# Performance work log

Hardware: AMD Instinct MI355X
Metric: run time of the kernel (lower is better)

Reference implementation:

```python
import jax, jax.numpy as jnp
import numpy as np

DIM = 512
HEADS = 8
DIM_HEAD = 64
INNER = HEADS * DIM_HEAD  # 512
PATCH = 64
M = 3
IN_CH = PATCH * PATCH // 2      # 2048
OUT_CH = IN_CH // 2             # 1024
B, N = 8, PATCH * PATCH // 4    # 8, 1024
SCALE = DIM_HEAD ** -0.5


def setup_inputs() -> dict:
    key = jax.random.key(0)
    ks = jax.random.split(key, 16)
    rn = lambda k, shp, s: (jax.random.normal(k, shp, dtype=jnp.float32) * s)
    inp = rn(ks[0], (B, N, DIM), 1.0)
    x = rn(ks[1], (B, N, DIM), 1.0)
    y = rn(ks[2], (B, N, DIM), 1.0)
    # Linear params (torch convention: W [out, in], y = x @ W.T + b)
    Wq = rn(ks[3], (INNER, DIM), DIM ** -0.5)
    bq = jnp.zeros((INNER,), jnp.float32)
    Wkv = rn(ks[4], (2 * INNER, DIM), DIM ** -0.5)
    bkv = jnp.zeros((2 * INNER,), jnp.float32)
    Wf = rn(ks[5], (OUT_CH + M, IN_CH + M), (IN_CH + M) ** -0.5)
    bf = jnp.zeros((OUT_CH + M,), jnp.float32)
    Wo = rn(ks[6], (DIM, INNER), INNER ** -0.5)
    bo = jnp.zeros((DIM,), jnp.float32)
    # memory tokens (xavier_normal std = sqrt(2/(m+inner)))
    std = np.sqrt(2.0 / (M + INNER))
    m_k = rn(ks[7], (1, M, INNER), std)
    m_v = rn(ks[8], (1, M, INNER), std)
    Sm_k = rn(ks[9], (1, M, INNER), std)
    Sm_v = rn(ks[10], (1, M, INNER), std)
    return dict(inp=inp, x=x, y=y, Wq=Wq, bq=bq, Wkv=Wkv, bkv=bkv,
                Wf=Wf, bf=bf, Wo=Wo, bo=bo,
                m_k=m_k, m_v=m_v, Sm_k=Sm_k, Sm_v=Sm_v)


def _split_heads(t):
    # 'b n (h d) -> b h n d'
    b, n, _ = t.shape
    return t.reshape(b, n, HEADS, DIM_HEAD).transpose(0, 2, 1, 3)


def _mem_view(p, b):
    # torch: p.expand(b, M, INNER).view(b, HEADS, M, DIM_HEAD) — raw reshape
    return jnp.broadcast_to(p, (b, M, INNER)).reshape(b, HEADS, M, DIM_HEAD)


def reference(inp, x, y, Wq, bq, Wkv, bkv, Wf, bf, Wo, bo, m_k, m_v, Sm_k, Sm_v):
    b = inp.shape[0]
    context = jnp.concatenate([x, y], axis=1)            # [b, 2n, dim]
    q = _split_heads(inp @ Wq.T + bq)                    # [b, h, n, d]
    kv = context @ Wkv.T + bkv
    k, v = jnp.split(kv, 2, axis=-1)
    k, v = _split_heads(k), _split_heads(v)              # [b, h, 2n, d]
    mk = np.sqrt(DIM_HEAD).astype(np.float32) * _mem_view(m_k, b)
    mv = np.sqrt(M).astype(np.float32) * _mem_view(m_v, b)
    k = jnp.concatenate([k, mk], axis=2)                 # [b, h, 2n+m, d]
    v = jnp.concatenate([v, mv], axis=2)
    dots = jnp.einsum('bhid,bhjd->bhij', q, k) * SCALE
    cross_attn = jax.nn.softmax(dots, axis=-1)           # [b, h, n, 2n+m]

    skv = inp @ Wkv.T + bkv
    S_k, S_v = jnp.split(skv, 2, axis=-1)
    S_k, S_v = _split_heads(S_k), _split_heads(S_v)      # [b, h, n, d]
    Smk = np.sqrt(DIM_HEAD).astype(np.float32) * _mem_view(Sm_k, b)
    Smv = np.sqrt(M).astype(np.float32) * _mem_view(Sm_v, b)
    Sk = jnp.concatenate([S_k, Smk], axis=2)             # [b, h, n+m, d]
    Sv = jnp.concatenate([S_v, Smv], axis=2)
    dots2 = jnp.einsum('bhid,bhjd->bhij', q, Sk) * SCALE
    self_attn = jax.nn.softmax(dots2, axis=-1)           # [b, h, n, n+m]

    cross_attn = cross_attn @ Wf.T + bf                  # [b, h, n, n+m]
    attn = cross_attn + self_attn
    out = jnp.einsum('bhij,bhjd->bhid', attn, Sv)        # [b, h, n, d]
    out = out.transpose(0, 2, 1, 3).reshape(b, -1, INNER)
    return out @ Wo.T + bo                               # [b, n, dim]
```

## Files before the change

kernel.cpp:

```cpp
#include <hip/hip_runtime.h>
#include <hip/hip_bf16.h>
#include <type_traits>

using bf16 = __hip_bfloat16;
typedef float f32x4 __attribute__((ext_vector_type(4)));
typedef __bf16 bf16x8_t __attribute__((ext_vector_type(8)));
typedef short  s16x8_t  __attribute__((ext_vector_type(8)));

template <typename V, typename = void> struct MfmaWorks : std::false_type {};
template <typename V>
struct MfmaWorks<V, std::void_t<decltype(__builtin_amdgcn_mfma_f32_16x16x32_bf16(
    std::declval<V>(), std::declval<V>(), std::declval<f32x4>(), 0, 0, 0))>> : std::true_type {};
using frag_t = std::conditional_t<MfmaWorks<bf16x8_t>::value, bf16x8_t, s16x8_t>;

template <typename V>
__device__ __forceinline__ f32x4 mfma_16x16x32(V a, V b, f32x4 c) {
    return __builtin_amdgcn_mfma_f32_16x16x32_bf16(a, b, c, 0, 0, 0);
}

__device__ __forceinline__ void gld_lds16(const void* g, void* l) {
    __builtin_amdgcn_global_load_lds(
        (const __attribute__((address_space(1))) unsigned int*)g,
        (__attribute__((address_space(3))) unsigned int*)l, 16, 0, 0);
}

__device__ __forceinline__ unsigned pack2(float lo, float hi) {
    bf16 a = __float2bfloat16(lo), b = __float2bfloat16(hi);
    unsigned short al, bl;
    __builtin_memcpy(&al, &a, 2);
    __builtin_memcpy(&bl, &b, 2);
    return (unsigned)al | ((unsigned)bl << 16);
}

__device__ __forceinline__ float ldin(const void* p, long i, int f32) {
    return f32 ? ((const float*)p)[i] : __bfloat162float(((const bf16*)p)[i]);
}

__global__ void detect_dtype(const void* __restrict__ inp, int* __restrict__ flag)
{
    const int t = threadIdx.x;
    int sane_cnt = 0;
#pragma unroll
    for (int s = 0; s < 4; s++) {
        float v = __bfloat162float(((const bf16*)inp)[2 * (t + 64 * s)]);
        float a = fabsf(v);
        bool sane = (a == 0.f) || (a > 9e-4f && a < 1000.f);
        unsigned long long m = __ballot(sane);
        sane_cnt += (int)__popcll(m);
    }
    if (t == 0) *flag = (sane_cnt > 128) ? 0 : 1;
}

__global__ __launch_bounds__(256)
void cvt_gen8(const void* __restrict__ src, long srcOff, bf16* __restrict__ dst,
              long nsrc, long ndst, const int* __restrict__ flag, float scale)
{
    const int f = *flag;
    const long i0 = ((long)blockIdx.x * 256 + threadIdx.x) * 8;
    if (i0 >= ndst) return;
#pragma unroll
    for (int u = 0; u < 8; u++) {
        const long i = i0 + u;
        if (i < ndst) dst[i] = __float2bfloat16(i < nsrc ? scale * ldin(src, srcOff + i, f) : 0.f);
    }
}

__global__ __launch_bounds__(256)
void cvt_weights(const void* __restrict__ Wq, const void* __restrict__ Wkv,
                 const void* __restrict__ Wo,
                 bf16* __restrict__ WqB, bf16* __restrict__ WkvB, bf16* __restrict__ WoB,
                 const int* __restrict__ flag, float qscale)
{
    const int f = *flag;
    long id = (long)blockIdx.x * 256 + threadIdx.x;
    const void* src; bf16* dst; float sc;
    if (blockIdx.x < 128)      { src = Wq;  dst = WqB;  sc = qscale; }
    else if (blockIdx.x < 384) { src = Wkv; dst = WkvB; sc = 1.f; id -= 128L * 256; }
    else                       { src = Wo;  dst = WoB;  sc = 1.f; id -= 384L * 256; }
    const long i0 = id * 8;
#pragma unroll
    for (int u = 0; u < 8; u++)
        dst[i0 + u] = __float2bfloat16(sc * ldin(src, i0 + u, f));
}

__global__ __launch_bounds__(256)
void cvt_small(const void* __restrict__ bq, const void* __restrict__ bkv,
               const void* __restrict__ bo, const void* __restrict__ mk,
               const void* __restrict__ Smk, const void* __restrict__ Smv,
               bf16* __restrict__ bqB, bf16* __restrict__ bkvB, bf16* __restrict__ boB,
               bf16* __restrict__ mkS, bf16* __restrict__ SmkS, bf16* __restrict__ SmvS,
               const int* __restrict__ flag, float qscale)
{
    const int f = *flag;
    const void* src; bf16* dst; int n; float sc;
    switch (blockIdx.x) {
        case 0:  src = bq;  dst = bqB;  n = 512;  sc = qscale;     break;
        case 1:  src = bkv; dst = bkvB; n = 1024; sc = 1.f;        break;
        case 2:  src = bo;  dst = boB;  n = 512;  sc = 1.f;        break;
        case 3:  src = mk;  dst = mkS;  n = 1536; sc = 8.f;        break;
        case 4:  src = Smk; dst = SmkS; n = 1536; sc = 8.f;        break;
        default: src = Smv; dst = SmvS; n = 1536; sc = 1.7320508f; break;
    }
    for (int i = threadIdx.x; i < n; i += 256)
        dst[i] = __float2bfloat16(sc * ldin(src, i, f));
}

__global__ __launch_bounds__(256)
void cvt_ctx8(const void* __restrict__ x, const void* __restrict__ y,
              bf16* __restrict__ ctx, const int* __restrict__ flag)
{
    const int f = *flag;
    const long i0 = ((long)blockIdx.x * 256 + threadIdx.x) * 8;
    const long r = i0 >> 9, c0 = i0 & 511;
    const long b = r >> 11, jj = r & 2047;
    const void* src = (jj < 1024) ? x : y;
    const long  soff = (jj < 1024) ? ((b * 1024 + jj) * 512 + c0)
                                   : ((b * 1024 + (jj - 1024)) * 512 + c0);
#pragma unroll
    for (int u = 0; u < 8; u++)
        ctx[i0 + u] = __float2bfloat16(ldin(src, soff + u, f));
}

__global__ __launch_bounds__(256)
void cvt_wft(const void* __restrict__ Wf, const void* __restrict__ bff,
             bf16* __restrict__ WfT, const int* __restrict__ flag)
{
    const int f = *flag;
    const long i0 = ((long)blockIdx.x * 256 + threadIdx.x) * 8;
    if (i0 >= 2176L * 1056) return;
    const long j = i0 / 1056, r0 = i0 % 1056;
    __align__(16) bf16 tmp[8];
#pragma unroll
    for (int u = 0; u < 8; u++) {
        const long r = r0 + u;
        float v = 0.f;
        if (r < 1027) {
            if (j < 2051)       v = ldin(Wf, r * 2051 + j, f);
            else if (j == 2051) v = ldin(bff, r, f);
        }
        tmp[u] = __float2bfloat16(v);
    }
    *(uint4*)(WfT + i0) = *(const uint4*)tmp;
}

__global__ __launch_bounds__(256)
void pack_k(const bf16* __restrict__ Ck, const bf16* __restrict__ mkS, bf16* __restrict__ kb)
{
    const long id = (long)blockIdx.x * 256 + threadIdx.x;
    const long bh = id / (2176 * 8);
    const long rem = id % (2176 * 8);
    const long j = rem >> 3;
    const long dg = (rem & 7) << 3;
    const long b = bh >> 3, h = bh & 7;
    bf16* dst = kb + (bh * 2176 + j) * 64 + dg;
    if (j < 2048) {
        *(uint4*)dst = *(const uint4*)(Ck + (b * 2048 + j) * 512 + h * 64 + dg);
    } else if (j < 2051) {
        *(uint4*)dst = *(const uint4*)(mkS + h * 192 + (j - 2048) * 64 + dg);
    } else {
        uint4 zz = {0, 0, 0, 0};
        *(uint4*)dst = zz;
    }
}

__global__ __launch_bounds__(256)
void pack_sk(const bf16* __restrict__ Cskv, const bf16* __restrict__ SmkS, bf16* __restrict__ Skb)
{
    const long id = (long)blockIdx.x * 256 + threadIdx.x;
    const long bh = id / (1152 * 8);
    const long rem = id % (1152 * 8);
    const long j = rem >> 3;
    const long dg = (rem & 7) << 3;
    const long b = bh >> 3, h = bh & 7;
    bf16* dst = Skb + (bh * 1152 + j) * 64 + dg;
    if (j < 1024) {
        *(uint4*)dst = *(const uint4*)(Cskv + (b * 1024 + j) * 1024 + h * 64 + dg);
    } else if (j < 1027) {
        *(uint4*)dst = *(const uint4*)(SmkS + h * 192 + (j - 1024) * 64 + dg);
    } else {
        uint4 zz = {0, 0, 0, 0};
        *(uint4*)dst = zz;
    }
}

__global__ __launch_bounds__(256)
void pack_svt(const bf16* __restrict__ Cskv, const bf16* __restrict__ SmvS,
              bf16* __restrict__ GTS, bf16* __restrict__ SvC)
{
    const long id = (long)blockIdx.x * 256 + threadIdx.x;
    const long bh = id / (128 * 132);
    const long rem = id % (128 * 132);
    const long dd = rem / 132;
    const long j0 = (rem % 132) << 3;
    const long b = bh >> 3, h = bh & 7;
    __align__(16) bf16 tmp[8];
#pragma unroll
    for (int u = 0; u < 8; u++) {
        const long j = j0 + u;
        float v = 0.f;
        if (dd < 64) {
            if (j < 1024)      v = __bfloat162float(Cskv[(b * 1024 + j) * 1024 + 512 + h * 64 + dd]);
            else if (j < 1027) v = __bfloat162float(SmvS[h * 192 + (j - 1024) * 64 + dd]);
        }
        tmp[u] = __float2bfloat16(v);
    }
    *(uint4*)(GTS + (bh * 128 + dd) * 3136 + 2080 + j0) = *(const uint4*)tmp;
    if (dd < 64)
        *(uint4*)(SvC + ((bh << 6) + dd) * 1056 + j0) = *(const uint4*)tmp;
}

__global__ __launch_bounds__(256)
void add2_cvt(const float* __restrict__ o0, const float* __restrict__ o1,
              bf16* __restrict__ outb)
{
    const long i0 = ((long)blockIdx.x * 256 + threadIdx.x) * 8;
    __align__(16) bf16 tmp[8];
#pragma unroll
    for (int u = 0; u < 8; u++)
        tmp[u] = __float2bfloat16(o0[i0 + u] + o1[i0 + u]);
    *(uint4*)(outb + i0) = *(const uint4*)tmp;
}

#define TM 128
#define TN 128
#define BK 32

template<int OMODE>
__global__ __launch_bounds__(256)
void gemm_nt(const bf16* __restrict__ A, long lda, long sAz,
             const bf16* __restrict__ B, long ldb, long sBz,
             void* __restrict__ Cv, long ldc, long sCz,
             int K,
             const bf16* __restrict__ bias,
             int validN, int zeroN,
             void* __restrict__ Cv2, long ldc2, int splitN)
{
    __shared__ __align__(16) short As[TM * BK];
    __shared__ __align__(16) short Bs[TN * BK];

    const int t = threadIdx.x;
    const int wave = t >> 6;
    const int lane = t & 63;
    const int bn = blockIdx.x, bm = blockIdx.y, z = blockIdx.z;

    const bf16* Ab = A + (long)z * sAz + (long)bm * TM * lda;
    const bf16* Bb = B + (long)z * sBz + (long)bn * TN * ldb;

    const int lrow = t >> 2;
    const int lcol = (t & 3) << 3;

    const f32x4 vzero = {0.f, 0.f, 0.f, 0.f};
    f32x4 acc[4][4];
#pragma unroll
    for (int i = 0; i < 4; i++)
#pragma unroll
        for (int j = 0; j < 4; j++) acc[i][j] = vzero;

    const int wr = (wave >> 1) << 6;
    const int wc = (wave & 1) << 6;
    const int fr = lane & 15;
    const int fq = (lane >> 4) << 3;

    for (int k0 = 0; k0 < K; k0 += BK) {
        __syncthreads();
        gld_lds16(Ab + (long)lrow * lda + (k0 + lcol),        (char*)As + wave * 1024);
        gld_lds16(Ab + (long)(64 + lrow) * lda + (k0 + lcol), (char*)As + 4096 + wave * 1024);
        gld_lds16(Bb + (long)lrow * ldb + (k0 + lcol),        (char*)Bs + wave * 1024);
        gld_lds16(Bb + (long)(64 + lrow) * ldb + (k0 + lcol), (char*)Bs + 4096 + wave * 1024);
        __builtin_amdgcn_s_waitcnt(0);
        __syncthreads();

        frag_t af[4], bfr[4];
#pragma unroll
        for (int i = 0; i < 4; i++) af[i]  = *(const frag_t*)&As[(wr + i * 16 + fr) * BK + fq];
#pragma unroll
        for (int j = 0; j < 4; j++) bfr[j] = *(const frag_t*)&Bs[(wc + j * 16 + fr) * BK + fq];
#pragma unroll
        for (int i = 0; i < 4; i++)
#pragma unroll
            for (int j = 0; j < 4; j++)
                acc[i][j] = mfma_16x16x32<frag_t>(af[i], bfr[j], acc[i][j]);
    }

    const int r0 = bm * TM + wr + ((lane >> 4) << 2);
    const int c0 = bn * TN + wc + fr;
    if (OMODE == 2) {
#pragma unroll
        for (int j = 0; j < 4; j++) {
            const int c = c0 + j * 16;
            bf16* rowp = (bf16*)Cv + ((long)(c >> 6) * 128 + (c & 63)) * 3136;
#pragma unroll
            for (int i = 0; i < 4; i++) {
                const int rgb = r0 + i * 16;
                if (rgb >= zeroN) continue;
                __align__(8) bf16 t4[4];
#pragma unroll
                for (int r = 0; r < 4; r++) t4[r] = __float2bfloat16(acc[i][j][r]);
                *(uint2*)(rowp + rgb) = *(const uint2*)t4;
            }
        }
        return;
    }
#pragma unroll
    for (int j = 0; j < 4; j++) {
        const int c = c0 + j * 16;
        if (c >= zeroN) continue;
        const bool valid = c < validN;
        float bv = 0.f;
        if (valid && bias) bv = __bfloat162float(bias[c]);
        bf16* obase = (bf16*)Cv; long old = ldc; int cc = c;
        if (OMODE == 0 && Cv2 && c >= splitN) { obase = (bf16*)Cv2; old = ldc2; cc = c - splitN; }
#pragma unroll
        for (int i = 0; i < 4; i++)
#pragma unroll
            for (int r = 0; r < 4; r++) {
                const long rg = r0 + i * 16 + r;
                if (OMODE == 1) {
                    ((float*)Cv)[(long)z * sCz + rg * ldc + c] = acc[i][j][r] + bv;
                } else {
                    float v = valid ? acc[i][j][r] + bv : 0.f;
                    obase[(long)z * sCz + rg * old + cc] = __float2bfloat16(v);
                }
            }
    }
}

__global__ __launch_bounds__(256, 4)
void attn_fused(const bf16* __restrict__ q,
                const bf16* __restrict__ kb,
                const bf16* __restrict__ Skb,
                const bf16* __restrict__ GTS,
                float* __restrict__ out0,
                float* __restrict__ out1)
{
    __shared__ __align__(16) bf16 Ks[2][64 * 64];
    __shared__ __align__(16) bf16 Gs[2][64 * 64];
    __shared__ __align__(16) unsigned Psw[4][16][32];

    const int t = threadIdx.x;
    const int w = t >> 6, lane = t & 63;
    const int bh = blockIdx.x, bm = blockIdx.y;
    const int phase = blockIdx.z;
    const int b = bh >> 3, h = bh & 7;
    const int g  = lane >> 4;
    const int fr = lane & 15;

    const bf16* Qg = q + ((long)(b * 1024 + bm * 128)) * 512 + h * 64;
    {
        const int qr = t >> 3, qc0 = (t & 7) << 3;
#pragma unroll
        for (int u = 0; u < 4; u++)
            gld_lds16(Qg + (long)(u * 32 + qr) * 512 + qc0, (char*)Ks + u * 4096 + w * 1024);
    }
    __builtin_amdgcn_s_waitcnt(0);
    __syncthreads();

    frag_t qf[2][2];
#pragma unroll
    for (int it = 0; it < 2; it++)
#pragma unroll
        for (int kh = 0; kh < 2; kh++)
            qf[it][kh] = *(const frag_t*)&((const bf16*)Ks)[(w * 32 + it * 16 + fr) * 64 + kh * 32 + g * 8];
    __syncthreads();

    union { frag_t f; short s[8]; } ou;
#pragma unroll
    for (int i = 0; i < 8; i++) ou.s[i] = 0x3F80;
    const frag_t onesf = ou.f;

    const f32x4 vzero = {0.f, 0.f, 0.f, 0.f};
    const int rs = t >> 3, gs = t & 7;
    const int glo = gs ^ (rs & 7);

    const bf16* Kb = phase ? Skb + (long)bh * 1152 * 64 : kb + (long)bh * 2176 * 64;
    const bf16* Gb = GTS + (long)bh * 128 * 3136 + (phase ? 2080 : 0);
    const int NC = phase ? 17 : 33;
    const int valid = phase ? 1027 : 2051;

    f32x4 oacc[2][4];
    f32x4 lacc[2];
#pragma unroll
    for (int it = 0; it < 2; it++) {
        lacc[it] = vzero;
#pragma unroll
        for (int dt = 0; dt < 4; dt++) oacc[it][dt] = vzero;
    }

    gld_lds16(Kb + (long)rs * 64 + glo * 8,          (char*)Ks[0] + w * 1024);
    gld_lds16(Kb + (long)(32 + rs) * 64 + glo * 8,   (char*)Ks[0] + 4096 + w * 1024);
    gld_lds16(Gb + (long)rs * 3136 + glo * 8,        (char*)Gs[0] + w * 1024);
    gld_lds16(Gb + (long)(32 + rs) * 3136 + glo * 8, (char*)Gs[0] + 4096 + w * 1024);

    unsigned* prow = &Psw[w][fr][0];
    const int swzk = (fr & 7) << 2;

    for (int c = 0; c < NC; c++) {
        const int buf = c & 1;
        __builtin_amdgcn_s_waitcnt(0);
        __syncthreads();
        if (c + 1 < NC) {
            const bf16* Kc = Kb + (long)(c + 1) * 64 * 64;
            const bf16* Gc = Gb + (c + 1) * 64;
            gld_lds16(Kc + (long)rs * 64 + glo * 8,          (char*)Ks[buf ^ 1] + w * 1024);
            gld_lds16(Kc + (long)(32 + rs) * 64 + glo * 8,   (char*)Ks[buf ^ 1] + 4096 + w * 1024);
            gld_lds16(Gc + (long)rs * 3136 + glo * 8,        (char*)Gs[buf ^ 1] + w * 1024);
            gld_lds16(Gc + (long)(32 + rs) * 3136 + glo * 8, (char*)Gs[buf ^ 1] + 4096 + w * 1024);
        }
        const bf16* Kl = Ks[buf];
        const bf16* Gl = Gs[buf];

        f32x4 s2[2][4];
#pragma unroll
        for (int it = 0; it < 2; it++)
#pragma unroll
            for (int ct = 0; ct < 4; ct++) s2[it][ct] = vzero;
        __builtin_amdgcn_s_setprio(1);
#pragma unroll
        for (int ct = 0; ct < 4; ct++)
#pragma unroll
            for (int kh = 0; kh < 2; kh++) {
                const int gph = (kh * 4 + g) ^ (fr & 7);
                const frag_t kf = *(const frag_t*)&Kl[(ct * 16 + fr) * 64 + gph * 8];
                s2[0][ct] = mfma_16x16x32<frag_t>(kf, qf[0][kh], s2[0][ct]);
                s2[1][ct] = mfma_16x16x32<frag_t>(kf, qf[1][kh], s2[1][ct]);
            }
        __builtin_amdgcn_s_setprio(0);

        if (c == NC - 1) {
#pragma unroll
            for (int ct = 0; ct < 4; ct++)
#pragma unroll
                for (int r = 0; r < 4; r++) {
                    const int kAbs = c * 64 + ct * 16 + 4 * g + r;
                    if (kAbs >= valid) { s2[0][ct][r] = -1.0e30f; s2[1][ct][r] = -1.0e30f; }
                }
        }

        frag_t pa[2][2];
#pragma unroll
        for (int it = 0; it < 2; it++) {
#pragma unroll
            for (int ct = 0; ct < 4; ct++) {
                const unsigned w0 = pack2(exp2f(s2[it][ct][0]), exp2f(s2[it][ct][1]));
                const unsigned w1 = pack2(exp2f(s2[it][ct][2]), exp2f(s2[it][ct][3]));
                *(uint2*)&prow[(ct * 8 + 2 * g) ^ swzk] = make_uint2(w0, w1);
            }
#pragma unroll
            for (int kh = 0; kh < 2; kh++)
                pa[it][kh] = *(const frag_t*)&prow[(kh * 16 + 4 * g) ^ swzk];
        }

        __builtin_amdgcn_s_setprio(1);
#pragma unroll
        for (int kh = 0; kh < 2; kh++) {
            lacc[0] = mfma_16x16x32<frag_t>(pa[0][kh], onesf, lacc[0]);
            lacc[1] = mfma_16x16x32<frag_t>(pa[1][kh], onesf, lacc[1]);
#pragma unroll
            for (int dt = 0; dt < 4; dt++) {
                const int gph = (kh * 4 + g) ^ (fr & 7);
                const frag_t gf = *(const frag_t*)&Gl[(dt * 16 + fr) * 64 + gph * 8];
                oacc[0][dt] = mfma_16x16x32<frag_t>(pa[0][kh], gf, oacc[0][dt]);
                oacc[1][dt] = mfma_16x16x32<frag_t>(pa[1][kh], gf, oacc[1][dt]);
            }
        }
        __builtin_amdgcn_s_setprio(0);
    }

    float gba[4] = {0.f, 0.f, 0.f, 0.f};
    if (phase == 0) {
        const bf16* gp = GTS + (long)bh * 128 * 3136 + 2051;
#pragma unroll
        for (int dt = 0; dt < 4; dt++)
            gba[dt] = __bfloat162float(gp[(long)(dt * 16 + fr) * 3136]);
    }
    float* Og = (phase ? out1 : out0) + ((long)(b * 1024 + bm * 128)) * 512 + h * 64;
#pragma unroll
    for (int it = 0; it < 2; it++)
#pragma unroll
        for (int r = 0; r < 4; r++) {
            const float inv = 1.f / lacc[it][r];
#pragma unroll
            for (int dt = 0; dt < 4; dt++) {
                Og[(long)(w * 32 + it * 16 + g * 4 + r) * 512 + dt * 16 + fr] =
                    oacc[it][dt][r] * inv + gba[dt];
            }
        }
}

extern "C" void kernel_launch(void* const* d_in, const int* in_sizes, int n_in,
                              void* d_out, int out_size, void* d_ws, size_t ws_size,
                              hipStream_t stream)
{
    const void* inp  = d_in[0];
    const void* x    = d_in[1];
    const void* y    = d_in[2];
    const void* Wq   = d_in[3];
    const void* bq   = d_in[4];
    const void* Wkv  = d_in[5];
    const void* bkv  = d_in[6];
    const void* Wf   = d_in[7];
    const void* bff  = d_in[8];
    const void* Wo   = d_in[9];
    const void* bo   = d_in[10];
    const void* m_k  = d_in[11];
    const void* Sm_k = d_in[13];
    const void* Sm_v = d_in[14];

    char* ws = (char*)d_ws;
    int*  flag = (int*)(ws + 0);
    bf16* WqB  = (bf16*)(ws + 256);
    bf16* WkvB = (bf16*)(ws + 524544);
    bf16* WoB  = (bf16*)(ws + 1573120);
    bf16* WfT  = (bf16*)(ws + 2097408);
    bf16* bqB  = (bf16*)(ws + 6693120);
    bf16* bkvB = (bf16*)(ws + 6694144);
    bf16* boB  = (bf16*)(ws + 6696192);
    bf16* mkS  = (bf16*)(ws + 6697216);
    bf16* SmkS = (bf16*)(ws + 6700288);
    bf16* SmvS = (bf16*)(ws + 6703360);
    bf16* qb   = (bf16*)(ws + 6706432);
    bf16* kb   = (bf16*)(ws + 15095040);
    bf16* Skb  = (bf16*)(ws + 32920832);
    bf16* GTS  = (bf16*)(ws + 42358016);
    bf16* outb = (bf16*)(ws + 93738240);
    char* OV   = ws + 102126848;

    bf16* inpB = (bf16*)(OV);
    bf16* Cskv = (bf16*)(OV + 8388608);
    bf16* ctxB = (bf16*)(OV);
    bf16* Ck   = (bf16*)(OV + 16777216);
    bf16* SvC  = (bf16*)(OV + 33554432);
    float* out0f = (float*)(OV);
    float* out1f = (float*)(OV + 16777216);

    const dim3 blk(256);
    const bf16* nulb = nullptr;
    const float QS = 0.125f * 1.44269504f;
    const int NOSPLIT = 1 << 30;

    detect_dtype<<<dim3(1), dim3(64), 0, stream>>>(inp, flag);

    cvt_weights<<<dim3(512), blk, 0, stream>>>(Wq, Wkv, Wo, WqB, WkvB, WoB, flag, QS);
    cvt_wft   <<<dim3(1122), blk, 0, stream>>>(Wf, bff, WfT, flag);
    cvt_small <<<dim3(6),    blk, 0, stream>>>(bq, bkv, bo, m_k, Sm_k, Sm_v,
                                               bqB, bkvB, boB, mkS, SmkS, SmvS, flag, QS);

    cvt_gen8<<<dim3(2048), blk, 0, stream>>>(inp, 0, inpB, 4194304, 4194304, flag, 1.f);
    gemm_nt<0><<<dim3(12, 64, 1), blk, 0, stream>>>(inpB, 512, 0, WqB, 512, 0, (void*)qb, 512, 0,
                                                    512, bqB, 1536, 1536,
                                                    (void*)Cskv, 1024, 512);
    pack_sk <<<dim3(2304), blk, 0, stream>>>(Cskv, SmkS, Skb);
    pack_svt<<<dim3(4224), blk, 0, stream>>>(Cskv, SmvS, GTS, SvC);
    gemm_nt<2><<<dim3(32, 17, 1), blk, 0, stream>>>(WfT, 1056, 0, SvC, 1056, 0,
                                                    (void*)GTS, 0, 0,
                                                    1056, nulb, 0, 2080,
                                                    nullptr, 0, NOSPLIT);
    cvt_ctx8<<<dim3(4096), blk, 0, stream>>>(x, y, ctxB, flag);
    gemm_nt<0><<<dim3(4, 128, 1), blk, 0, stream>>>(ctxB, 512, 0, WkvB, 512, 0, (void*)Ck, 512, 0,
                                                    512, bkvB, 512, 512,
                                                    nullptr, 0, NOSPLIT);
    pack_k<<<dim3(4352), blk, 0, stream>>>(Ck, mkS, kb);

    attn_fused<<<dim3(64, 8, 2), blk, 0, stream>>>(qb, kb, Skb, GTS, out0f, out1f);
    add2_cvt<<<dim3(2048), blk, 0, stream>>>(out0f, out1f, outb);

    gemm_nt<1><<<dim3(4, 64, 1), blk, 0, stream>>>(outb, 512, 0, WoB, 512, 0, d_out, 512, 0,
                                                   512, boB, 512, 512,
                                                   nullptr, 0, NOSPLIT);
}
```

Before: 394.9 us.

## Fuse packing and add into GEMM epilogues/prologues and merge prep kernels

Merges all weight, bias and memory-token conversion kernels into one prep launch that writes the memory-token rows straight into the packed K/Sk/GTS/SvC buffers. The QKV and context GEMMs gain epilogue modes that scatter results directly into the head-split packed layouts, which removes the pack_k, pack_sk and pack_svt passes. The output GEMM reads both fp32 attention partials, adds them and converts to bf16 in its A-load, which removes add2_cvt. This cuts kernel launches and intermediate global round-trips. The cost is scattered, non-coalesced epilogue stores and a synchronous A-load path in the last GEMM in place of the async LDS load.

```diff
diff --git a/kernel.cpp b/kernel.cpp
--- a/kernel.cpp
+++ b/kernel.cpp
@@ -52,57 +52,109 @@
 }
 
 __global__ __launch_bounds__(256)
-void cvt_gen8(const void* __restrict__ src, long srcOff, bf16* __restrict__ dst,
-              long nsrc, long ndst, const int* __restrict__ flag, float scale)
+void cvt_gen8(const void* __restrict__ src, bf16* __restrict__ dst,
+              long ndst, const int* __restrict__ flag, float scale)
 {
     const int f = *flag;
     const long i0 = ((long)blockIdx.x * 256 + threadIdx.x) * 8;
     if (i0 >= ndst) return;
 #pragma unroll
-    for (int u = 0; u < 8; u++) {
-        const long i = i0 + u;
-        if (i < ndst) dst[i] = __float2bfloat16(i < nsrc ? scale * ldin(src, srcOff + i, f) : 0.f);
-    }
+    for (int u = 0; u < 8; u++)
+        dst[i0 + u] = __float2bfloat16(scale * ldin(src, i0 + u, f));
 }
 
 __global__ __launch_bounds__(256)
-void cvt_weights(const void* __restrict__ Wq, const void* __restrict__ Wkv,
-                 const void* __restrict__ Wo,
-                 bf16* __restrict__ WqB, bf16* __restrict__ WkvB, bf16* __restrict__ WoB,
-                 const int* __restrict__ flag, float qscale)
+void prep(const void* __restrict__ Wq, const void* __restrict__ Wkv,
+          const void* __restrict__ Wo, const void* __restrict__ Wf,
+          const void* __restrict__ bff, const void* __restrict__ bq,
+          const void* __restrict__ bkv, const void* __restrict__ bo,
+          const void* __restrict__ mk, const void* __restrict__ Smk,
+          const void* __restrict__ Smv,
+          bf16* __restrict__ WqB, bf16* __restrict__ WkvB, bf16* __restrict__ WoB,
+          bf16* __restrict__ WfT, bf16* __restrict__ bqB, bf16* __restrict__ bkvB,
+          bf16* __restrict__ boB, bf16* __restrict__ kb, bf16* __restrict__ Skb,
+          bf16* __restrict__ GTS, bf16* __restrict__ SvC,
+          const int* __restrict__ flag, float qscale)
 {
     const int f = *flag;
-    long id = (long)blockIdx.x * 256 + threadIdx.x;
-    const void* src; bf16* dst; float sc;
-    if (blockIdx.x < 128)      { src = Wq;  dst = WqB;  sc = qscale; }
-    else if (blockIdx.x < 384) { src = Wkv; dst = WkvB; sc = 1.f; id -= 128L * 256; }
-    else                       { src = Wo;  dst = WoB;  sc = 1.f; id -= 384L * 256; }
-    const long i0 = id * 8;
-#pragma unroll
-    for (int u = 0; u < 8; u++)
-        dst[i0 + u] = __float2bfloat16(sc * ldin(src, i0 + u, f));
-}
-
-__global__ __launch_bounds__(256)
-void cvt_small(const void* __restrict__ bq, const void* __restrict__ bkv,
-               const void* __restrict__ bo, const void* __restrict__ mk,
-               const void* __restrict__ Smk, const void* __restrict__ Smv,
-               bf16* __restrict__ bqB, bf16* __restrict__ bkvB, bf16* __restrict__ boB,
-               bf16* __restrict__ mkS, bf16* __restrict__ SmkS, bf16* __restrict__ SmvS,
-               const int* __restrict__ flag, float qscale)
-{
-    const int f = *flag;
-    const void* src; bf16* dst; int n; float sc;
-    switch (blockIdx.x) {
-        case 0:  src = bq;  dst = bqB;  n = 512;  sc = qscale;     break;
-        case 1:  src = bkv; dst = bkvB; n = 1024; sc = 1.f;        break;
-        case 2:  src = bo;  dst = boB;  n = 512;  sc = 1.f;        break;
-        case 3:  src = mk;  dst = mkS;  n = 1536; sc = 8.f;        break;
-        case 4:  src = Smk; dst = SmkS; n = 1536; sc = 8.f;        break;
-        default: src = Smv; dst = SmvS; n = 1536; sc = 1.7320508f; break;
-    }
-    for (int i = threadIdx.x; i < n; i += 256)
-        dst[i] = __float2bfloat16(sc * ldin(src, i, f));
+    const int blk = blockIdx.x;
+    const int t = threadIdx.x;
+    const float SQRT3 = 1.7320508f;
+
+    if (blk < 512) {
+        long id = (long)blk * 256 + t;
+        const void* src; bf16* dst; float sc;
+        if (blk < 128)      { src = Wq;  dst = WqB;  sc = qscale; }
+        else if (blk < 384) { src = Wkv; dst = WkvB; sc = 1.f; id -= 128L * 256; }
+        else                { src = Wo;  dst = WoB;  sc = 1.f; id -= 384L * 256; }
+        const long i0 = id * 8;
+#pragma unroll
+        for (int u = 0; u < 8; u++)
+            dst[i0 + u] = __float2bfloat16(sc * ldin(src, i0 + u, f));
+    } else if (blk < 1634) {
+        const long i0 = ((long)(blk - 512) * 256 + t) * 8;
+        if (i0 >= 2176L * 1056) return;
+        const long j = i0 / 1056, r0 = i0 % 1056;
+        __align__(16) bf16 tmp[8];
+#pragma unroll
+        for (int u = 0; u < 8; u++) {
+            const long r = r0 + u;
+            float v = 0.f;
+            if (r < 1027) {
+                if (j < 2051)       v = ldin(Wf, r * 2051 + j, f);
+                else if (j == 2051) v = ldin(bff, r, f);
+            }
+            tmp[u] = __float2bfloat16(v);
+        }
+        *(uint4*)(WfT + i0) = *(const uint4*)tmp;
+    } else if (blk < 1637) {
+        const void* src; bf16* dst; int n; float sc;
+        switch (blk - 1634) {
+            case 0:  src = bq;  dst = bqB;  n = 512;  sc = qscale; break;
+            case 1:  src = bkv; dst = bkvB; n = 1024; sc = 1.f;    break;
+            default: src = bo;  dst = boB;  n = 512;  sc = 1.f;    break;
+        }
+        for (int i = t; i < n; i += 256)
+            dst[i] = __float2bfloat16(sc * ldin(src, i, f));
+    } else if (blk < 1893) {
+        const long e = ((long)(blk - 1637) * 256 + t) * 8;
+        const long bh = e >> 13, rem = e & 8191;
+        const long jj = rem >> 6, dg0 = rem & 63;
+        const long h = bh & 7;
+        __align__(16) bf16 tmp[8];
+#pragma unroll
+        for (int u = 0; u < 8; u++) {
+            float v = (jj < 3) ? 8.f * ldin(mk, jj * 512 + h * 64 + dg0 + u, f) : 0.f;
+            tmp[u] = __float2bfloat16(v);
+        }
+        *(uint4*)(kb + (bh * 2176 + 2048 + jj) * 64 + dg0) = *(const uint4*)tmp;
+    } else if (blk < 2149) {
+        const long e = ((long)(blk - 1893) * 256 + t) * 8;
+        const long bh = e >> 13, rem = e & 8191;
+        const long jj = rem >> 6, dg0 = rem & 63;
+        const long h = bh & 7;
+        __align__(16) bf16 tmp[8];
+#pragma unroll
+        for (int u = 0; u < 8; u++) {
+            float v = (jj < 3) ? 8.f * ldin(Smk, jj * 512 + h * 64 + dg0 + u, f) : 0.f;
+            tmp[u] = __float2bfloat16(v);
+        }
+        *(uint4*)(Skb + (bh * 1152 + 1024 + jj) * 64 + dg0) = *(const uint4*)tmp;
+    } else {
+        const long e = ((long)(blk - 2149) * 256 + t) * 8;
+        const long bh = e >> 11, rem = e & 2047;
+        const long dd = rem >> 5, jc0 = rem & 31;
+        const long h = bh & 7;
+        __align__(16) bf16 tmp[8];
+#pragma unroll
+        for (int u = 0; u < 8; u++) {
+            const long jc = jc0 + u;
+            float v = (jc < 3) ? SQRT3 * ldin(Smv, jc * 512 + h * 64 + dd, f) : 0.f;
+            tmp[u] = __float2bfloat16(v);
+        }
+        *(uint4*)(GTS + (bh * 128 + dd) * 3136 + 3104 + jc0) = *(const uint4*)tmp;
+        *(uint4*)(SvC + (bh * 64 + dd) * 1056 + 1024 + jc0)  = *(const uint4*)tmp;
+    }
 }
 
 __global__ __launch_bounds__(256)
@@ -119,106 +171,6 @@
 #pragma unroll
     for (int u = 0; u < 8; u++)
         ctx[i0 + u] = __float2bfloat16(ldin(src, soff + u, f));
-}
-
-__global__ __launch_bounds__(256)
-void cvt_wft(const void* __restrict__ Wf, const void* __restrict__ bff,
-             bf16* __restrict__ WfT, const int* __restrict__ flag)
-{
-    const int f = *flag;
-    const long i0 = ((long)blockIdx.x * 256 + threadIdx.x) * 8;
-    if (i0 >= 2176L * 1056) return;
-    const long j = i0 / 1056, r0 = i0 % 1056;
-    __align__(16) bf16 tmp[8];
-#pragma unroll
-    for (int u = 0; u < 8; u++) {
-        const long r = r0 + u;
-        float v = 0.f;
-        if (r < 1027) {
-            if (j < 2051)       v = ldin(Wf, r * 2051 + j, f);
-            else if (j == 2051) v = ldin(bff, r, f);
-        }
-        tmp[u] = __float2bfloat16(v);
-    }
-    *(uint4*)(WfT + i0) = *(const uint4*)tmp;
-}
-
-__global__ __launch_bounds__(256)
-void pack_k(const bf16* __restrict__ Ck, const bf16* __restrict__ mkS, bf16* __restrict__ kb)
-{
-    const long id = (long)blockIdx.x * 256 + threadIdx.x;
-    const long bh = id / (2176 * 8);
-    const long rem = id % (2176 * 8);
-    const long j = rem >> 3;
-    const long dg = (rem & 7) << 3;
-    const long b = bh >> 3, h = bh & 7;
-    bf16* dst = kb + (bh * 2176 + j) * 64 + dg;
-    if (j < 2048) {
-        *(uint4*)dst = *(const uint4*)(Ck + (b * 2048 + j) * 512 + h * 64 + dg);
-    } else if (j < 2051) {
-        *(uint4*)dst = *(const uint4*)(mkS + h * 192 + (j - 2048) * 64 + dg);
-    } else {
-        uint4 zz = {0, 0, 0, 0};
-        *(uint4*)dst = zz;
-    }
-}
-
-__global__ __launch_bounds__(256)
-void pack_sk(const bf16* __restrict__ Cskv, const bf16* __restrict__ SmkS, bf16* __restrict__ Skb)
-{
-    const long id = (long)blockIdx.x * 256 + threadIdx.x;
-    const long bh = id / (1152 * 8);
-    const long rem = id % (1152 * 8);
-    const long j = rem >> 3;
-    const long dg = (rem & 7) << 3;
-    const long b = bh >> 3, h = bh & 7;
-    bf16* dst = Skb + (bh * 1152 + j) * 64 + dg;
-    if (j < 1024) {
-        *(uint4*)dst = *(const uint4*)(Cskv + (b * 1024 + j) * 1024 + h * 64 + dg);
-    } else if (j < 1027) {
-        *(uint4*)dst = *(const uint4*)(SmkS + h * 192 + (j - 1024) * 64 + dg);
-    } else {
-        uint4 zz = {0, 0, 0, 0};
-        *(uint4*)dst = zz;
-    }
-}
-
-__global__ __launch_bounds__(256)
-void pack_svt(const bf16* __restrict__ Cskv, const bf16* __restrict__ SmvS,
-              bf16* __restrict__ GTS, bf16* __restrict__ SvC)
-{
-    const long id = (long)blockIdx.x * 256 + threadIdx.x;
-    const long bh = id / (128 * 132);
-    const long rem = id % (128 * 132);
-    const long dd = rem / 132;
-    const long j0 = (rem % 132) << 3;
-    const long b = bh >> 3, h = bh & 7;
-    __align__(16) bf16 tmp[8];
-#pragma unroll
-    for (int u = 0; u < 8; u++) {
-        const long j = j0 + u;
-        float v = 0.f;
-        if (dd < 64) {
-            if (j < 1024)      v = __bfloat162float(Cskv[(b * 1024 + j) * 1024 + 512 + h * 64 + dd]);
-            else if (j < 1027) v = __bfloat162float(SmvS[h * 192 + (j - 1024) * 64 + dd]);
-        }
-        tmp[u] = __float2bfloat16(v);
-    }
-    *(uint4*)(GTS + (bh * 128 + dd) * 3136 + 2080 + j0) = *(const uint4*)tmp;
-    if (dd < 64)
-        *(uint4*)(SvC + ((bh << 6) + dd) * 1056 + j0) = *(const uint4*)tmp;
-}
-
-__global__ __launch_bounds__(256)
-void add2_cvt(const float* __restrict__ o0, const float* __restrict__ o1,
-              bf16* __restrict__ outb)
-{
-    const long i0 = ((long)blockIdx.x * 256 + threadIdx.x) * 8;
-    __align__(16) bf16 tmp[8];
-#pragma unroll
-    for (int u = 0; u < 8; u++)
-        tmp[u] = __float2bfloat16(o0[i0 + u] + o1[i0 + u]);
-    *(uint4*)(outb + i0) = *(const uint4*)tmp;
 }
 
 #define TM 128
@@ -233,7 +185,7 @@
              int K,
              const bf16* __restrict__ bias,
              int validN, int zeroN,
-             void* __restrict__ Cv2, long ldc2, int splitN)
+             void* __restrict__ Cv2, void* __restrict__ Cv3, void* __restrict__ Cv4)
 {
     __shared__ __align__(16) short As[TM * BK];
     __shared__ __align__(16) short Bs[TN * BK];
@@ -263,8 +215,27 @@
 
     for (int k0 = 0; k0 < K; k0 += BK) {
         __syncthreads();
-        gld_lds16(Ab + (long)lrow * lda + (k0 + lcol),        (char*)As + wave * 1024);
-        gld_lds16(Ab + (long)(64 + lrow) * lda + (k0 + lcol), (char*)As + 4096 + wave * 1024);
+        if constexpr (OMODE == 5) {
+            const int ar = t >> 1;
+            const int ac = (t & 1) << 4;
+            const float* a0 = (const float*)A   + (long)(bm * TM + ar) * lda + k0 + ac;
+            const float* a1 = (const float*)Cv2 + (long)(bm * TM + ar) * lda + k0 + ac;
+            __align__(16) bf16 tt[16];
+#pragma unroll
+            for (int u = 0; u < 4; u++) {
+                const float4 v0 = *(const float4*)(a0 + u * 4);
+                const float4 v1 = *(const float4*)(a1 + u * 4);
+                tt[u * 4 + 0] = __float2bfloat16(v0.x + v1.x);
+                tt[u * 4 + 1] = __float2bfloat16(v0.y + v1.y);
+                tt[u * 4 + 2] = __float2bfloat16(v0.z + v1.z);
+                tt[u * 4 + 3] = __float2bfloat16(v0.w + v1.w);
+            }
+            *(uint4*)&As[ar * BK + ac]     = *(const uint4*)&tt[0];
+            *(uint4*)&As[ar * BK + ac + 8] = *(const uint4*)&tt[8];
+        } else {
+            gld_lds16(Ab + (long)lrow * lda + (k0 + lcol),        (char*)As + wave * 1024);
+            gld_lds16(Ab + (long)(64 + lrow) * lda + (k0 + lcol), (char*)As + 4096 + wave * 1024);
+        }
         gld_lds16(Bb + (long)lrow * ldb + (k0 + lcol),        (char*)Bs + wave * 1024);
         gld_lds16(Bb + (long)(64 + lrow) * ldb + (k0 + lcol), (char*)Bs + 4096 + wave * 1024);
         __builtin_amdgcn_s_waitcnt(0);
@@ -284,7 +255,8 @@
 
     const int r0 = bm * TM + wr + ((lane >> 4) << 2);
     const int c0 = bn * TN + wc + fr;
-    if (OMODE == 2) {
+
+    if constexpr (OMODE == 2) {
 #pragma unroll
         for (int j = 0; j < 4; j++) {
             const int c = c0 + j * 16;
@@ -301,26 +273,76 @@
         }
         return;
     }
+    if constexpr (OMODE == 3) {
+        const int bb = bm >> 3;
+#pragma unroll
+        for (int j = 0; j < 4; j++) {
+            const int c = c0 + j * 16;
+            const float bv = __bfloat162float(bias[c]);
+            if (c < 512) {
+#pragma unroll
+                for (int i = 0; i < 4; i++)
+#pragma unroll
+                    for (int r = 0; r < 4; r++) {
+                        const long rg = r0 + i * 16 + r;
+                        ((bf16*)Cv)[rg * ldc + c] = __float2bfloat16(acc[i][j][r] + bv);
+                    }
+            } else if (c < 1024) {
+                const int h = (c - 512) >> 6, dg = c & 63;
+                bf16* base = (bf16*)Cv2 + ((long)(bb * 8 + h) * 1152) * 64 + dg;
+#pragma unroll
+                for (int i = 0; i < 4; i++)
+#pragma unroll
+                    for (int r = 0; r < 4; r++) {
+                        const long jj = (r0 + i * 16 + r) & 1023;
+                        base[jj * 64] = __float2bfloat16(acc[i][j][r] + bv);
+                    }
+            } else {
+                const int h = (c - 1024) >> 6, dd = c & 63;
+                bf16* svt = (bf16*)Cv3 + ((long)(bb * 8 + h) * 128 + dd) * 3136 + 2080;
+                bf16* svc = (bf16*)Cv4 + ((long)(bb * 8 + h) * 64 + dd) * 1056;
+#pragma unroll
+                for (int i = 0; i < 4; i++) {
+                    const long j0 = (r0 + i * 16) & 1023;
+                    __align__(8) bf16 t4[4];
+#pragma unroll
+                    for (int r = 0; r < 4; r++) t4[r] = __float2bfloat16(acc[i][j][r] + bv);
+                    *(uint2*)(svt + j0) = *(const uint2*)t4;
+                    *(uint2*)(svc + j0) = *(const uint2*)t4;
+                }
+            }
+        }
+        return;
+    }
+    if constexpr (OMODE == 4) {
+        const int bb = bm >> 4;
+#pragma unroll
+        for (int j = 0; j < 4; j++) {
+            const int c = c0 + j * 16;
+            const float bv = __bfloat162float(bias[c]);
+            const int h = c >> 6, dg = c & 63;
+            bf16* base = (bf16*)Cv + ((long)(bb * 8 + h) * 2176) * 64 + dg;
+#pragma unroll
+            for (int i = 0; i < 4; i++)
+#pragma unroll
+                for (int r = 0; r < 4; r++) {
+                    const long jj = (r0 + i * 16 + r) & 2047;
+                    base[jj * 64] = __float2bfloat16(acc[i][j][r] + bv);
+                }
+        }
+        return;
+    }
 #pragma unroll
     for (int j = 0; j < 4; j++) {
         const int c = c0 + j * 16;
         if (c >= zeroN) continue;
-        const bool valid = c < validN;
-        float bv = 0.f;
-        if (valid && bias) bv = __bfloat162float(bias[c]);
-        bf16* obase = (bf16*)Cv; long old = ldc; int cc = c;
-        if (OMODE == 0 && Cv2 && c >= splitN) { obase = (bf16*)Cv2; old = ldc2; cc = c - splitN; }
+        const float bv = bias ? __bfloat162float(bias[c]) : 0.f;
 #pragma unroll
         for (int i = 0; i < 4; i++)
 #pragma unroll
             for (int r = 0; r < 4; r++) {
                 const long rg = r0 + i * 16 + r;
-                if (OMODE == 1) {
-                    ((float*)Cv)[(long)z * sCz + rg * ldc + c] = acc[i][j][r] + bv;
-                } else {
-                    float v = valid ? acc[i][j][r] + bv : 0.f;
-                    obase[(long)z * sCz + rg * old + cc] = __float2bfloat16(v);
-                }
+                ((float*)Cv)[(long)z * sCz + rg * ldc + c] = acc[i][j][r] + bv;
             }
     }
 }
@@ -515,56 +537,44 @@
     bf16* bqB  = (bf16*)(ws + 6693120);
     bf16* bkvB = (bf16*)(ws + 6694144);
     bf16* boB  = (bf16*)(ws + 6696192);
-    bf16* mkS  = (bf16*)(ws + 6697216);
-    bf16* SmkS = (bf16*)(ws + 6700288);
-    bf16* SmvS = (bf16*)(ws + 6703360);
     bf16* qb   = (bf16*)(ws + 6706432);
     bf16* kb   = (bf16*)(ws + 15095040);
     bf16* Skb  = (bf16*)(ws + 32920832);
     bf16* GTS  = (bf16*)(ws + 42358016);
-    bf16* outb = (bf16*)(ws + 93738240);
-    char* OV   = ws + 102126848;
-
-    bf16* inpB = (bf16*)(OV);
-    bf16* Cskv = (bf16*)(OV + 8388608);
-    bf16* ctxB = (bf16*)(OV);
-    bf16* Ck   = (bf16*)(OV + 16777216);
-    bf16* SvC  = (bf16*)(OV + 33554432);
+    char* OV   = ws + 93738240;
+
+    bf16*  inpB  = (bf16*)(OV);
+    bf16*  SvC   = (bf16*)(OV + 16777216);
+    bf16*  ctxB  = (bf16*)(OV);
     float* out0f = (float*)(OV);
     float* out1f = (float*)(OV + 16777216);
 
     const dim3 blk(256);
     const bf16* nulb = nullptr;
     const float QS = 0.125f * 1.44269504f;
-    const int NOSPLIT = 1 << 30;
 
     detect_dtype<<<dim3(1), dim3(64), 0, stream>>>(inp, flag);
 
-    cvt_weights<<<dim3(512), blk, 0, stream>>>(Wq, Wkv, Wo, WqB, WkvB, WoB, flag, QS);
-    cvt_wft   <<<dim3(1122), blk, 0, stream>>>(Wf, bff, WfT, flag);
-    cvt_small <<<dim3(6),    blk, 0, stream>>>(bq, bkv, bo, m_k, Sm_k, Sm_v,
-                                               bqB, bkvB, boB, mkS, SmkS, SmvS, flag, QS);
-
-    cvt_gen8<<<dim3(2048), blk, 0, stream>>>(inp, 0, inpB, 4194304, 4194304, flag, 1.f);
-    gemm_nt<0><<<dim3(12, 64, 1), blk, 0, stream>>>(inpB, 512, 0, WqB, 512, 0, (void*)qb, 512, 0,
-                                                    512, bqB, 1536, 1536,
-                                                    (void*)Cskv, 1024, 512);
-    pack_sk <<<dim3(2304), blk, 0, stream>>>(Cskv, SmkS, Skb);
-    pack_svt<<<dim3(4224), blk, 0, stream>>>(Cskv, SmvS, GTS, SvC);
+    prep<<<dim3(2213), blk, 0, stream>>>(Wq, Wkv, Wo, Wf, bff, bq, bkv, bo,
+                                         m_k, Sm_k, Sm_v,
+                                         WqB, WkvB, WoB, WfT, bqB, bkvB, boB,
+                                         kb, Skb, GTS, SvC, flag, QS);
+
+    cvt_gen8<<<dim3(2048), blk, 0, stream>>>(inp, inpB, 4194304, flag, 1.f);
+
+    gemm_nt<3><<<dim3(12, 64, 1), blk, 0, stream>>>(inpB, 512, 0, WqB, 512, 0,
+        (void*)qb, 512, 0, 512, bqB, 1536, 1536, (void*)Skb, (void*)GTS, (void*)SvC);
+
     gemm_nt<2><<<dim3(32, 17, 1), blk, 0, stream>>>(WfT, 1056, 0, SvC, 1056, 0,
-                                                    (void*)GTS, 0, 0,
-                                                    1056, nulb, 0, 2080,
-                                                    nullptr, 0, NOSPLIT);
+        (void*)GTS, 0, 0, 1056, nulb, 0, 2080, nullptr, nullptr, nullptr);
+
     cvt_ctx8<<<dim3(4096), blk, 0, stream>>>(x, y, ctxB, flag);
-    gemm_nt<0><<<dim3(4, 128, 1), blk, 0, stream>>>(ctxB, 512, 0, WkvB, 512, 0, (void*)Ck, 512, 0,
-                                                    512, bkvB, 512, 512,
-                                                    nullptr, 0, NOSPLIT);
-    pack_k<<<dim3(4352), blk, 0, stream>>>(Ck, mkS, kb);
+
+    gemm_nt<4><<<dim3(4, 128, 1), blk, 0, stream>>>(ctxB, 512, 0, WkvB, 512, 0,
+        (void*)kb, 0, 0, 512, bkvB, 512, 512, nullptr, nullptr, nullptr);
 
     attn_fused<<<dim3(64, 8, 2), blk, 0, stream>>>(qb, kb, Skb, GTS, out0f, out1f);
-    add2_cvt<<<dim3(2048), blk, 0, stream>>>(out0f, out1f, outb);
-
-    gemm_nt<1><<<dim3(4, 64, 1), blk, 0, stream>>>(outb, 512, 0, WoB, 512, 0, d_out, 512, 0,
-                                                   512, boB, 512, 512,
-                                                   nullptr, 0, NOSPLIT);
-}
+
+    gemm_nt<5><<<dim3(4, 64, 1), blk, 0, stream>>>((const bf16*)out0f, 512, 0, WoB, 512, 0,
+        d_out, 512, 0, 512, boB, 512, 512, (void*)out1f, nullptr, nullptr);
+}
```

New measurement: 359.9 us. 8.9% less time.
